# Optimization experiments

Hardware: AMD Instinct MI355X
Metric: run time of the kernel (lower is better)

The kernel has to match this reference:

```python
import jax, jax.numpy as jnp
import numpy as np

N_REAL = 1_000_000
C_IN = 32
C_OUT = 32
PAD = 1_050_000


def setup_inputs() -> dict:
    key = jax.random.key(0)
    k_x, k_fn, k_w0, k_w1, k_w2, k_b = jax.random.split(key, 6)
    x = jax.random.normal(k_x, (N_REAL, C_IN), dtype=jnp.float32)
    face_neighborhood = jax.random.randint(k_fn, (N_REAL, 9), 0, PAD, dtype=jnp.int32)
    # real faces occupy the first N_REAL padded slots; the rest are pads
    face_is_pad = jnp.arange(PAD) >= N_REAL
    # kaiming-uniform-style init for [out, in] weights (fan_in = C_IN for 1x1 taps)
    bw = 1.0 / np.sqrt(C_IN)
    w0 = jax.random.uniform(k_w0, (C_OUT, C_IN), jnp.float32, -bw, bw)
    w1 = jax.random.uniform(k_w1, (C_OUT, C_IN), jnp.float32, -bw, bw)
    w2 = jax.random.uniform(k_w2, (C_OUT, C_IN), jnp.float32, -bw, bw)
    bb = 1.0 / np.sqrt(C_IN * 9)  # fan_in of the full (out,in,1,9) kernel
    bias = jax.random.uniform(k_b, (C_OUT,), jnp.float32, -bb, bb)
    return {"x": x, "w0": w0, "w1": w1, "w2": w2, "bias": bias,
            "face_neighborhood": face_neighborhood, "face_is_pad": face_is_pad,
            "pad_size": PAD}


def reference(x, w0, w1, w2, bias, face_neighborhood, face_is_pad, pad_size):
    # Scatter x into padded buffer: padded_x[~face_is_pad] = x (jit-safe via cumsum map)
    keep = jnp.logical_not(face_is_pad)
    src = jnp.cumsum(keep.astype(jnp.int32)) - 1  # index into x for each kept slot
    padded_x = jnp.where(keep[:, None], x[jnp.clip(src, 0, x.shape[0] - 1)],
                         jnp.zeros((), x.dtype))  # [pad_size, C]
    # Symmetric 1x9 filter = [w0, w1, w2, w1, w2, w1, w2, w1, w2]:
    # fold the 9 gathers into 3 groups before the tiny GEMMs.
    g0 = padded_x[face_neighborhood[:, 0]]
    g1 = (padded_x[face_neighborhood[:, 1]] + padded_x[face_neighborhood[:, 3]]
          + padded_x[face_neighborhood[:, 5]] + padded_x[face_neighborhood[:, 7]])
    g2 = (padded_x[face_neighborhood[:, 2]] + padded_x[face_neighborhood[:, 4]]
          + padded_x[face_neighborhood[:, 6]] + padded_x[face_neighborhood[:, 8]])
    out = (jnp.einsum('nc,oc->no', g0, w0)
           + jnp.einsum('nc,oc->no', g1, w1)
           + jnp.einsum('nc,oc->no', g2, w2)
           + bias)
    return out
```

## Files before the change

kernel.cpp:

```cpp
#include <hip/hip_runtime.h>
#include <hip/hip_fp16.h>

typedef _Float16 half8 __attribute__((ext_vector_type(8)));
typedef _Float16 half4v __attribute__((ext_vector_type(4)));
typedef float float4v __attribute__((ext_vector_type(4)));

#define BLOCK 256
#define ROWS_PER_BLOCK 64
#define ROWPITCH 104

__device__ _Float16 g_wh[6 * 512];

__global__ void prep_weights(const float* __restrict__ w0,
                             const float* __restrict__ w1,
                             const float* __restrict__ w2) {
    const int t = threadIdx.x;
    const int st = t >> 6;
    const int lane = t & 63;
    const int s = st >> 1, tt = st & 1;
    const float* w = (s == 0) ? w0 : (s == 1) ? w1 : w2;
    const int o = tt * 16 + (lane & 15);
    const int k = (lane >> 4) * 8;
    #pragma unroll
    for (int j = 0; j < 8; ++j)
        g_wh[st * 512 + lane * 8 + j] = (_Float16)w[o * 32 + k + j];
}

__global__ __launch_bounds__(BLOCK) void face_conv_kernel(
    const float* __restrict__ x,
    const float* __restrict__ bias,
    const int* __restrict__ fn,
    float* __restrict__ out,
    int N)
{
    __shared__ _Float16 A[4][16 * ROWPITCH];

    const int tid  = threadIdx.x;
    const int wave = tid >> 6;
    const int lane = tid & 63;
    const int m16  = lane & 15;
    const int quad = lane >> 4;
    const int oct  = lane >> 3;
    const int m8   = lane & 7;

    half8 bfrag[3][2];
    #pragma unroll
    for (int s = 0; s < 3; ++s)
        #pragma unroll
        for (int t = 0; t < 2; ++t)
            bfrag[s][t] = *(const half8*)(g_wh + (s * 2 + t) * 512 + lane * 8);
    const float bias0 = bias[m16];
    const float bias1 = bias[16 + m16];

    const int base = blockIdx.x * ROWS_PER_BLOCK + wave * 16;
    _Float16* Aw = A[wave];

    int idx[2][9];
    #pragma unroll
    for (int it = 0; it < 2; ++it) {
        int r = base + it * 8 + oct;
        r = (r < N) ? r : (N - 1);
        const int* fr = fn + (long)r * 9;
        #pragma unroll
        for (int j = 0; j < 9; ++j) idx[it][j] = __builtin_nontemporal_load(fr + j);
    }

    #pragma unroll
    for (int it = 0; it < 2; ++it) {
        float4v v[9];
        #pragma unroll
        for (int j = 0; j < 9; ++j) {
            const int id = idx[it][j];
            if ((unsigned)id < (unsigned)N) {
                v[j] = *(const float4v*)(x + (long)id * 32 + m8 * 4);
            } else {
                v[j] = (float4v){0.f, 0.f, 0.f, 0.f};
            }
        }
        const float4v g0 = v[0];
        const float4v g1 = v[1] + v[3] + v[5] + v[7];
        const float4v g2 = v[2] + v[4] + v[6] + v[8];
        _Float16* dst = Aw + (it * 8 + oct) * ROWPITCH + m8 * 4;
        *(half4v*)(dst)      = (half4v){(_Float16)g0.x, (_Float16)g0.y, (_Float16)g0.z, (_Float16)g0.w};
        *(half4v*)(dst + 32) = (half4v){(_Float16)g1.x, (_Float16)g1.y, (_Float16)g1.z, (_Float16)g1.w};
        *(half4v*)(dst + 64) = (half4v){(_Float16)g2.x, (_Float16)g2.y, (_Float16)g2.z, (_Float16)g2.w};
    }

    __syncthreads();

    float4v acc0 = {0.f, 0.f, 0.f, 0.f}, acc1 = {0.f, 0.f, 0.f, 0.f};
    #pragma unroll
    for (int s = 0; s < 3; ++s) {
        half8 a = *(half8*)(Aw + m16 * ROWPITCH + s * 32 + quad * 8);
        acc0 = __builtin_amdgcn_mfma_f32_16x16x32_f16(a, bfrag[s][0], acc0, 0, 0, 0);
        acc1 = __builtin_amdgcn_mfma_f32_16x16x32_f16(a, bfrag[s][1], acc1, 0, 0, 0);
    }

    #pragma unroll
    for (int i = 0; i < 4; ++i) {
        const int r = base + quad * 4 + i;
        if (r < N) {
            __builtin_nontemporal_store(acc0[i] + bias0, &out[(long)r * 32 + m16]);
            __builtin_nontemporal_store(acc1[i] + bias1, &out[(long)r * 32 + 16 + m16]);
        }
    }
}

extern "C" void kernel_launch(void* const* d_in, const int* in_sizes, int n_in,
                              void* d_out, int out_size, void* d_ws, size_t ws_size,
                              hipStream_t stream) {
    const float* x    = (const float*)d_in[0];
    const float* w0   = (const float*)d_in[1];
    const float* w1   = (const float*)d_in[2];
    const float* w2   = (const float*)d_in[3];
    const float* bias = (const float*)d_in[4];
    const int*   fn   = (const int*)d_in[5];
    float* out = (float*)d_out;

    const int N = in_sizes[0] / 32;
    const int blocks = (N + ROWS_PER_BLOCK - 1) / ROWS_PER_BLOCK;

    prep_weights<<<1, 384, 0, stream>>>(w0, w1, w2);
    face_conv_kernel<<<blocks, BLOCK, 0, stream>>>(x, bias, fn, out, N);
}
```

Measured before the change: 377.3 us.

## Pre-convert x to fp16 in workspace and gather half-precision rows

Adds a prep pass that converts x to fp16 in the workspace buffer. The conv kernel then gathers 64-byte fp16 rows instead of 128-byte fp32 rows and sums the nine neighbours in fp16. This halves the bytes moved by the random gathers, at the cost of an extra streaming pass over x and lower accumulation precision for the neighbour sums. It falls back to the fp32 path if the workspace is too small.

```diff
diff --git a/kernel.cpp b/kernel.cpp
--- a/kernel.cpp
+++ b/kernel.cpp
@@ -26,7 +26,95 @@
         g_wh[st * 512 + lane * 8 + j] = (_Float16)w[o * 32 + k + j];
 }
 
-__global__ __launch_bounds__(BLOCK) void face_conv_kernel(
+__global__ __launch_bounds__(256) void prep_x(const float* __restrict__ x,
+                                              _Float16* __restrict__ xh,
+                                              int total) {
+    const int i = (blockIdx.x * 256 + threadIdx.x) * 8;
+    if (i < total) {
+        float4v a = __builtin_nontemporal_load((const float4v*)(x + i));
+        float4v b = __builtin_nontemporal_load((const float4v*)(x + i + 4));
+        half8 h = {(_Float16)a.x, (_Float16)a.y, (_Float16)a.z, (_Float16)a.w,
+                   (_Float16)b.x, (_Float16)b.y, (_Float16)b.z, (_Float16)b.w};
+        *(half8*)(xh + i) = h;
+    }
+}
+
+__global__ __launch_bounds__(BLOCK) void face_conv_f16(
+    const _Float16* __restrict__ xh,
+    const float* __restrict__ bias,
+    const int* __restrict__ fn,
+    float* __restrict__ out,
+    int N)
+{
+    __shared__ _Float16 A[4][16 * ROWPITCH];
+
+    const int tid  = threadIdx.x;
+    const int wave = tid >> 6;
+    const int lane = tid & 63;
+    const int m16  = lane & 15;
+    const int quad = lane >> 4;
+    const int rloc = lane >> 2;
+    const int m4   = lane & 3;
+
+    half8 bfrag[3][2];
+    #pragma unroll
+    for (int s = 0; s < 3; ++s)
+        #pragma unroll
+        for (int t = 0; t < 2; ++t)
+            bfrag[s][t] = *(const half8*)(g_wh + (s * 2 + t) * 512 + lane * 8);
+    const float bias0 = bias[m16];
+    const float bias1 = bias[16 + m16];
+
+    const int base = blockIdx.x * ROWS_PER_BLOCK + wave * 16;
+    _Float16* Aw = A[wave];
+
+    int r = base + rloc;
+    if (r >= N) r = N - 1;
+    const int* fr = fn + (long)r * 9;
+    int idx[9];
+    #pragma unroll
+    for (int j = 0; j < 9; ++j) idx[j] = __builtin_nontemporal_load(fr + j);
+
+    half8 v[9];
+    #pragma unroll
+    for (int j = 0; j < 9; ++j) {
+        const int id = idx[j];
+        if ((unsigned)id < (unsigned)N) {
+            v[j] = *(const half8*)(xh + (long)id * 32 + m4 * 8);
+        } else {
+            v[j] = (half8){0, 0, 0, 0, 0, 0, 0, 0};
+        }
+    }
+    const half8 g0 = v[0];
+    const half8 g1 = (v[1] + v[3]) + (v[5] + v[7]);
+    const half8 g2 = (v[2] + v[4]) + (v[6] + v[8]);
+
+    _Float16* dst = Aw + rloc * ROWPITCH + m4 * 8;
+    *(half8*)(dst)      = g0;
+    *(half8*)(dst + 32) = g1;
+    *(half8*)(dst + 64) = g2;
+
+    __syncthreads();
+
+    float4v acc0 = {0.f, 0.f, 0.f, 0.f}, acc1 = {0.f, 0.f, 0.f, 0.f};
+    #pragma unroll
+    for (int s = 0; s < 3; ++s) {
+        half8 a = *(half8*)(Aw + m16 * ROWPITCH + s * 32 + quad * 8);
+        acc0 = __builtin_amdgcn_mfma_f32_16x16x32_f16(a, bfrag[s][0], acc0, 0, 0, 0);
+        acc1 = __builtin_amdgcn_mfma_f32_16x16x32_f16(a, bfrag[s][1], acc1, 0, 0, 0);
+    }
+
+    #pragma unroll
+    for (int i = 0; i < 4; ++i) {
+        const int rr = base + quad * 4 + i;
+        if (rr < N) {
+            __builtin_nontemporal_store(acc0[i] + bias0, &out[(long)rr * 32 + m16]);
+            __builtin_nontemporal_store(acc1[i] + bias1, &out[(long)rr * 32 + 16 + m16]);
+        }
+    }
+}
+
+__global__ __launch_bounds__(BLOCK) void face_conv_f32(
     const float* __restrict__ x,
     const float* __restrict__ bias,
     const int* __restrict__ fn,
@@ -34,7 +122,6 @@
     int N)
 {
     __shared__ _Float16 A[4][16 * ROWPITCH];
-
     const int tid  = threadIdx.x;
     const int wave = tid >> 6;
     const int lane = tid & 63;
@@ -64,18 +151,14 @@
         #pragma unroll
         for (int j = 0; j < 9; ++j) idx[it][j] = __builtin_nontemporal_load(fr + j);
     }
-
     #pragma unroll
     for (int it = 0; it < 2; ++it) {
         float4v v[9];
         #pragma unroll
         for (int j = 0; j < 9; ++j) {
             const int id = idx[it][j];
-            if ((unsigned)id < (unsigned)N) {
-                v[j] = *(const float4v*)(x + (long)id * 32 + m8 * 4);
-            } else {
-                v[j] = (float4v){0.f, 0.f, 0.f, 0.f};
-            }
+            if ((unsigned)id < (unsigned)N) v[j] = *(const float4v*)(x + (long)id * 32 + m8 * 4);
+            else                            v[j] = (float4v){0.f, 0.f, 0.f, 0.f};
         }
         const float4v g0 = v[0];
         const float4v g1 = v[1] + v[3] + v[5] + v[7];
@@ -85,7 +168,6 @@
         *(half4v*)(dst + 32) = (half4v){(_Float16)g1.x, (_Float16)g1.y, (_Float16)g1.z, (_Float16)g1.w};
         *(half4v*)(dst + 64) = (half4v){(_Float16)g2.x, (_Float16)g2.y, (_Float16)g2.z, (_Float16)g2.w};
     }
-
     __syncthreads();
 
     float4v acc0 = {0.f, 0.f, 0.f, 0.f}, acc1 = {0.f, 0.f, 0.f, 0.f};
@@ -95,13 +177,12 @@
         acc0 = __builtin_amdgcn_mfma_f32_16x16x32_f16(a, bfrag[s][0], acc0, 0, 0, 0);
         acc1 = __builtin_amdgcn_mfma_f32_16x16x32_f16(a, bfrag[s][1], acc1, 0, 0, 0);
     }
-
     #pragma unroll
     for (int i = 0; i < 4; ++i) {
-        const int r = base + quad * 4 + i;
-        if (r < N) {
-            __builtin_nontemporal_store(acc0[i] + bias0, &out[(long)r * 32 + m16]);
-            __builtin_nontemporal_store(acc1[i] + bias1, &out[(long)r * 32 + 16 + m16]);
+        const int rr = base + quad * 4 + i;
+        if (rr < N) {
+            __builtin_nontemporal_store(acc0[i] + bias0, &out[(long)rr * 32 + m16]);
+            __builtin_nontemporal_store(acc1[i] + bias1, &out[(long)rr * 32 + 16 + m16]);
         }
     }
 }
@@ -117,9 +198,19 @@
     const int*   fn   = (const int*)d_in[5];
     float* out = (float*)d_out;
 
-    const int N = in_sizes[0] / 32;
+    const int total = in_sizes[0];
+    const int N = total / 32;
     const int blocks = (N + ROWS_PER_BLOCK - 1) / ROWS_PER_BLOCK;
 
     prep_weights<<<1, 384, 0, stream>>>(w0, w1, w2);
-    face_conv_kernel<<<blocks, BLOCK, 0, stream>>>(x, bias, fn, out, N);
-}
+
+    const size_t xh_bytes = (size_t)total * sizeof(_Float16);
+    if (ws_size >= xh_bytes) {
+        _Float16* xh = (_Float16*)d_ws;
+        const int pblocks = (total / 8 + 255) / 256;
+        prep_x<<<pblocks, 256, 0, stream>>>(x, xh, total);
+        face_conv_f16<<<blocks, BLOCK, 0, stream>>>(xh, bias, fn, out, N);
+    } else {
+        face_conv_f32<<<blocks, BLOCK, 0, stream>>>(x, bias, fn, out, N);
+    }
+}
```

Result: slower. 399.7 us (+5.9%).
